# Kernel optimization log

Hardware: AMD Instinct MI355X
Metric: run time of the kernel (lower is better)

## Reference

```python
import jax, jax.numpy as jnp
import numpy as np

B, S, H, I, E, K = 1, 2048, 1024, 512, 16, 4


def setup_inputs() -> dict:
    key = jax.random.key(0)
    k0, k1, k2, k3, k4, k5 = jax.random.split(key, 6)
    hidden_states = jax.random.normal(k0, (B, S, H), jnp.float32)
    T = B * S
    topk_idx = jax.random.randint(k1, (T, K), 0, E, dtype=jnp.int32)
    raw = jax.random.uniform(k2, (T, K), jnp.float32)
    topk_weight = raw / jnp.sum(raw, axis=-1, keepdims=True)  # normalized top-k gate weights
    scale = 0.02
    w_gate = jax.random.normal(k3, (E, H, I), jnp.float32) * scale
    w_up = jax.random.normal(k4, (E, H, I), jnp.float32) * scale
    w_down = jax.random.normal(k5, (E, I, H), jnp.float32) * scale
    return {
        "hidden_states": hidden_states,
        "topk_idx": topk_idx,
        "topk_weight": topk_weight,
        "w_gate": w_gate,
        "w_up": w_up,
        "w_down": w_down,
    }


def reference(hidden_states, topk_idx, topk_weight, w_gate, w_up, w_down):
    # hidden_states: [B,S,H]; topk_idx/topk_weight: [T,K]; w_*: [E,H,I]/[E,I,H]
    b, s, h = hidden_states.shape
    t = b * s
    e = w_gate.shape[0]
    x = hidden_states.reshape(t, h)
    # routing_weights.scatter_(1, topk_idx, topk_weight)
    routing_weights = jnp.zeros((t, e), x.dtype).at[
        jnp.arange(t)[:, None], topk_idx
    ].set(topk_weight)
    # per-expert gated MLP over all tokens (math identical to masked dispatch:
    # tokens with routing weight 0 contribute nothing)
    g = jnp.einsum("th,ehi->eti", x, w_gate)  # [E,T,I]
    u = jnp.einsum("th,ehi->eti", x, w_up)
    d = jnp.einsum("eti,eih->eth", jax.nn.silu(g) * u, w_down)  # [E,T,H]
    out = jnp.einsum("eth,te->th", d, routing_weights)  # weighted combine
    return out.reshape(b, s, h)
```

## Files before the change

kernel.cpp:

```cpp
#include <hip/hip_runtime.h>
#include <hip/hip_bf16.h>
#include <stdint.h>

#define HH 1024
#define II 512
#define EE 16
#define TT 2048
#define KTOP 4
#define PP (TT * KTOP)
#define MAXROWS 12288

typedef unsigned short u16;
typedef unsigned int u32;
typedef __attribute__((ext_vector_type(8))) short short8;
typedef __attribute__((ext_vector_type(4))) float f32x4;
typedef __attribute__((ext_vector_type(4))) unsigned short u16x4;
typedef __attribute__((ext_vector_type(8))) unsigned short u16x8;
typedef __attribute__((ext_vector_type(4))) unsigned int u32x4;

__device__ __forceinline__ u16 f2bf(float f) {
  union { float f; unsigned u; } v; v.f = f;
  unsigned r = v.u + 0x7fffu + ((v.u >> 16) & 1u);
  return (u16)(r >> 16);
}
__device__ __forceinline__ float bf2f(u16 b) {
  union { unsigned u; float f; } v; v.u = ((unsigned)b) << 16; return v.f;
}
__device__ __forceinline__ u32 packbf(float lo, float hi) {
  return (u32)f2bf(lo) | ((u32)f2bf(hi) << 16);
}

__device__ __forceinline__ void gld16(const u16* g, u16* l) {
  __builtin_amdgcn_global_load_lds(
      (const __attribute__((address_space(1))) unsigned int*)g,
      (__attribute__((address_space(3))) unsigned int*)l, 16, 0, 0);
}

union PLds {
  int s_e[PP];
  u32 t32[2][128][68];
};

__global__ __launch_bounds__(1024) void prep_fused(
    const float* __restrict__ x, const int* __restrict__ tidx,
    const float* __restrict__ tw,
    const float* __restrict__ wg, const float* __restrict__ wu,
    u16* __restrict__ xb, u16* __restrict__ WgT, u16* __restrict__ WuT,
    int* __restrict__ perm, float* __restrict__ wt, int* __restrict__ rowof,
    int* __restrict__ tile_e, int* __restrict__ tile_r,
    int* __restrict__ ntiles) {
  __shared__ PLds L;
  __shared__ int whist[16][16];
  __shared__ int wbase[16][16];
  __shared__ int pad_lo[EE], pad_hi[EE];

  const int bid = blockIdx.x;
  const int tid = threadIdx.x;

  if (bid == 0) {
    const int lane = tid & 63;
    const int wv = tid >> 6;

#pragma unroll
    for (int i = 0; i < 2; i++) {
      const int t = tid + i * 1024;
      const int4 v = ((const int4*)tidx)[t];
      const bool v0 = (v.x != v.y) && (v.x != v.z) && (v.x != v.w);
      const bool v1 = (v.y != v.z) && (v.y != v.w);
      const bool v2 = (v.z != v.w);
      L.s_e[t * 4 + 0] = v.x | (v0 ? 16 : 0);
      L.s_e[t * 4 + 1] = v.y | (v1 ? 16 : 0);
      L.s_e[t * 4 + 2] = v.z | (v2 ? 16 : 0);
      L.s_e[t * 4 + 3] = v.w | 16;
    }
    __syncthreads();

    int h0, h1, h2, h3, h4, h5, h6, h7, h8, h9, h10, h11, h12, h13, h14, h15;
    h0=h1=h2=h3=h4=h5=h6=h7=h8=h9=h10=h11=h12=h13=h14=h15=0;
    const unsigned long long ltm = (1ull << lane) - 1ull;
    for (int c = 0; c < 8; c++) {
      const int p = (wv << 9) + (c << 6) + lane;
      const int se = L.s_e[p];
      const int e = se & 15;
      const bool valid = (se & 16) != 0;
      int rank = 0;
#define RANK_STEP(J, HJ)                                            \
      {                                                             \
        unsigned long long m = __ballot(valid && (e == J));         \
        if (valid && (e == J)) rank = HJ + __popcll(m & ltm);       \
        HJ += __popcll(m);                                          \
      }
      RANK_STEP(0, h0)  RANK_STEP(1, h1)  RANK_STEP(2, h2)  RANK_STEP(3, h3)
      RANK_STEP(4, h4)  RANK_STEP(5, h5)  RANK_STEP(6, h6)  RANK_STEP(7, h7)
      RANK_STEP(8, h8)  RANK_STEP(9, h9)  RANK_STEP(10, h10) RANK_STEP(11, h11)
      RANK_STEP(12, h12) RANK_STEP(13, h13) RANK_STEP(14, h14) RANK_STEP(15, h15)
#undef RANK_STEP
      if (valid) L.s_e[p] = se | (rank << 16);
    }
    if (lane == 0) {
      whist[wv][0] = h0;   whist[wv][1] = h1;   whist[wv][2] = h2;   whist[wv][3] = h3;
      whist[wv][4] = h4;   whist[wv][5] = h5;   whist[wv][6] = h6;   whist[wv][7] = h7;
      whist[wv][8] = h8;   whist[wv][9] = h9;   whist[wv][10] = h10; whist[wv][11] = h11;
      whist[wv][12] = h12; whist[wv][13] = h13; whist[wv][14] = h14; whist[wv][15] = h15;
    }
    __syncthreads();

    if (tid == 0) {
      int off = 0, nt = 0;
      for (int j = 0; j < EE; j++) {
        int tot = 0;
        for (int w = 0; w < 16; w++) { wbase[w][j] = off + tot; tot += whist[w][j]; }
        const int cap = (tot + 127) & ~127;
        pad_lo[j] = off + tot;
        pad_hi[j] = off + cap;
        for (int m0 = 0; m0 < cap; m0 += 128) { tile_e[nt] = j; tile_r[nt] = off + m0; nt++; }
        off += cap;
      }
      *ntiles = nt;
    }
    __syncthreads();

#pragma unroll
    for (int i = 0; i < 8; i++) {
      const int p = i * 1024 + tid;
      const int se = L.s_e[p];
      int pos = -1;
      if (se & 16) {
        const int e = se & 15;
        const int r = se >> 16;
        pos = wbase[p >> 9][e] + r;
        perm[pos] = p >> 2;
        wt[pos] = tw[p];
      }
      rowof[p] = pos;
    }
    for (int j = 0; j < EE; j++) {
      const int lo = pad_lo[j], hi = pad_hi[j];
      for (int i = lo + tid; i < hi; i += 1024) {
        perm[i] = 0;
        wt[i] = 0.f;
      }
    }
    return;
  }

  if (bid <= 128) {
    const int base = ((bid - 1) * 1024 + tid) * 16;
    f32x4 v0 = *(const f32x4*)(x + base);
    f32x4 v1 = *(const f32x4*)(x + base + 4);
    f32x4 v2 = *(const f32x4*)(x + base + 8);
    f32x4 v3 = *(const f32x4*)(x + base + 12);
    u16x8 o0 = { f2bf(v0[0]), f2bf(v0[1]), f2bf(v0[2]), f2bf(v0[3]),
                 f2bf(v1[0]), f2bf(v1[1]), f2bf(v1[2]), f2bf(v1[3]) };
    u16x8 o1 = { f2bf(v2[0]), f2bf(v2[1]), f2bf(v2[2]), f2bf(v2[3]),
                 f2bf(v3[0]), f2bf(v3[1]), f2bf(v3[2]), f2bf(v3[3]) };
    *(u16x8*)(xb + base) = o0;
    *(u16x8*)(xb + base + 8) = o1;
    return;
  }

  const int pb = bid - 129;
  const int zz = pb >> 5;
  const int sub = pb & 31;
  const int xi = sub & 3, yi = sub >> 2;
  const size_t mat = (size_t)zz * HH * II;
  const int r0 = yi * 128, c0 = xi * 128;

  const int rp = tid >> 4, cq8 = (tid & 15) * 8;
  const size_t soff = mat + (size_t)(r0 + 2 * rp) * II + c0 + cq8;
  const float* sp0 = wg + soff;
  const float* sp1 = wu + soff;
  const f32x4 a0 = *(const f32x4*)(sp0);
  const f32x4 a1 = *(const f32x4*)(sp0 + 4);
  const f32x4 b0 = *(const f32x4*)(sp0 + II);
  const f32x4 b1 = *(const f32x4*)(sp0 + II + 4);
  const f32x4 e0 = *(const f32x4*)(sp1);
  const f32x4 e1 = *(const f32x4*)(sp1 + 4);
  const f32x4 g0 = *(const f32x4*)(sp1 + II);
  const f32x4 g1 = *(const f32x4*)(sp1 + II + 4);
  __builtin_amdgcn_sched_barrier(0);

  const int key = tid & 15;
  const int rpx = rp ^ ((key & 7) << 3) ^ (((key >> 2) & 1) << 2);
  const int c = tid >> 3, q = tid & 7;
  const int rkey = c >> 3;
  const int qb = (q ^ (rkey & 7)) * 8;
  const int b2 = ((rkey >> 2) & 1) * 4;
  const size_t doff = mat + (size_t)(c0 + c) * HH + r0 + q * 16;

#pragma unroll
  for (int j = 0; j < 4; j++) L.t32[0][cq8 + j][rpx] = packbf(a0[j], b0[j]);
#pragma unroll
  for (int j = 0; j < 4; j++) L.t32[0][cq8 + 4 + j][rpx] = packbf(a1[j], b1[j]);
  __syncthreads();
#pragma unroll
  for (int j = 0; j < 4; j++) L.t32[1][cq8 + j][rpx] = packbf(e0[j], g0[j]);
#pragma unroll
  for (int j = 0; j < 4; j++) L.t32[1][cq8 + 4 + j][rpx] = packbf(e1[j], g1[j]);
  {
    u32x4 v0, v1;
#pragma unroll
    for (int j = 0; j < 4; j++) v0[j] = L.t32[0][c][qb + b2 + j];
#pragma unroll
    for (int j = 0; j < 4; j++) v1[j] = L.t32[0][c][qb + (b2 ^ 4) + j];
    u16* dp = WgT + doff;
    *(u32x4*)(dp) = v0;
    *(u32x4*)(dp + 8) = v1;
  }
  __syncthreads();
  {
    u32x4 v0, v1;
#pragma unroll
    for (int j = 0; j < 4; j++) v0[j] = L.t32[1][c][qb + b2 + j];
#pragma unroll
    for (int j = 0; j < 4; j++) v1[j] = L.t32[1][c][qb + (b2 ^ 4) + j];
    u16* dp = WuT + doff;
    *(u32x4*)(dp) = v0;
    *(u32x4*)(dp + 8) = v1;
  }
}

__global__ __launch_bounds__(256) void gemm1_kernel(
    const u16* __restrict__ xb, const u16* __restrict__ WgT, const u16* __restrict__ WuT,
    const float* __restrict__ wd, u16* __restrict__ WdT,
    const int* __restrict__ perm, const float* __restrict__ wt,
    const int* __restrict__ tile_e, const int* __restrict__ tile_r,
    const int* __restrict__ ntiles, u16* __restrict__ ACT) {
  __shared__ __align__(16) u16 SMEM[16384];
  const int tid = threadIdx.x;

  if (blockIdx.y >= 80) {
    const int pb = (blockIdx.y - 80) * 8 + blockIdx.x;
    const int zz = pb >> 6;
    const int sub = pb & 63;
    const int r0 = (sub >> 4) * 128;
    const int c0 = (sub & 15) * 64;
    const size_t mat = (size_t)zz * II * HH;
    u32 (*T32)[68] = (u32(*)[68])SMEM;

    const int rpA = tid >> 3;
    const int cq8 = (tid & 7) * 8;
    const float* spA = wd + mat + (size_t)(r0 + 2 * rpA) * HH + c0 + cq8;
    const float* spB = spA + (size_t)64 * HH;
    const f32x4 a0 = *(const f32x4*)(spA);
    const f32x4 a1 = *(const f32x4*)(spA + 4);
    const f32x4 b0 = *(const f32x4*)(spA + HH);
    const f32x4 b1 = *(const f32x4*)(spA + HH + 4);
    const f32x4 e0 = *(const f32x4*)(spB);
    const f32x4 e1 = *(const f32x4*)(spB + 4);
    const f32x4 g0 = *(const f32x4*)(spB + HH);
    const f32x4 g1 = *(const f32x4*)(spB + HH + 4);
    __builtin_amdgcn_sched_barrier(0);

    const int key = tid & 7;
    const int sw = ((key & 7) << 3) ^ (((key >> 2) & 1) << 2);
    const int rpxA = rpA ^ sw;
    const int rpxB = (rpA + 32) ^ sw;
#pragma unroll
    for (int j = 0; j < 4; j++) T32[cq8 + j][rpxA] = packbf(a0[j], b0[j]);
#pragma unroll
    for (int j = 0; j < 4; j++) T32[cq8 + 4 + j][rpxA] = packbf(a1[j], b1[j]);
#pragma unroll
    for (int j = 0; j < 4; j++) T32[cq8 + j][rpxB] = packbf(e0[j], g0[j]);
#pragma unroll
    for (int j = 0; j < 4; j++) T32[cq8 + 4 + j][rpxB] = packbf(e1[j], g1[j]);
    __syncthreads();

    const int c = tid >> 2;
    const int q2 = tid & 3;
    const int rkey = c >> 3;
    const int b2 = ((rkey >> 2) & 1) * 4;
#pragma unroll
    for (int pass = 0; pass < 2; pass++) {
      const int o = q2 + pass * 4;
      const int qb = (o ^ (rkey & 7)) * 8;
      u32x4 v0, v1;
#pragma unroll
      for (int j = 0; j < 4; j++) v0[j] = T32[c][qb + b2 + j];
#pragma unroll
      for (int j = 0; j < 4; j++) v1[j] = T32[c][qb + (b2 ^ 4) + j];
      u16* dp = WdT + mat + (size_t)(c0 + c) * II + r0 + o * 16;
      *(u32x4*)(dp) = v0;
      *(u32x4*)(dp + 8) = v1;
    }
    return;
  }

  const int tileid = blockIdx.y;
  if (tileid >= *ntiles) return;
  const int e = tile_e[tileid];
  const int row0 = tile_r[tileid];
  const int n0 = blockIdx.x * 64;

  u16* const As = SMEM;
  u16* const Gs = SMEM + 8192;
  u16* const Us = SMEM + 12288;

  const int lane = tid & 63;
  const int wid = tid >> 6;
  const int wm = wid >> 1, wn = wid & 1;
  const int fr = lane & 15, fq = lane >> 4;

  const int lrow = lane >> 3;
  const int sc8 = ((lane & 7) ^ lrow) * 8;

  const u16* gA[4]; u16* lA[4];
#pragma unroll
  for (int j = 0; j < 4; j++) {
    const int trow = j * 32 + wid * 8 + lrow;
    gA[j] = xb + (size_t)perm[row0 + trow] * HH + sc8;
    lA[j] = As + (j * 4 + wid) * 512;
  }
  const u16 *gG[2], *gU[2];
  u16 *lG[2], *lU[2];
#pragma unroll
  for (int j = 0; j < 2; j++) {
    const int nrow = j * 32 + wid * 8 + lrow;
    gG[j] = WgT + ((size_t)e * II + n0 + nrow) * HH + sc8;
    gU[j] = WuT + ((size_t)e * II + n0 + nrow) * HH + sc8;
    lG[j] = Gs + (j * 4 + wid) * 512;
    lU[j] = Us + (j * 4 + wid) * 512;
  }

  f32x4 accg[4][2], accu[4][2];
  const f32x4 vz = {0.f, 0.f, 0.f, 0.f};
#pragma unroll
  for (int m = 0; m < 4; m++)
#pragma unroll
    for (int n = 0; n < 2; n++) { accg[m][n] = vz; accu[m][n] = vz; }

  for (int k0 = 0; k0 < HH; k0 += 64) {
    __syncthreads();
#pragma unroll
    for (int j = 0; j < 4; j++) gld16(gA[j] + k0, lA[j]);
#pragma unroll
    for (int j = 0; j < 2; j++) { gld16(gG[j] + k0, lG[j]); gld16(gU[j] + k0, lU[j]); }
    __syncthreads();

#pragma unroll
    for (int ks = 0; ks < 2; ks++) {
      short8 af[4], bg[2], bu[2];
#pragma unroll
      for (int m = 0; m < 4; m++) {
        const int r = wm * 64 + m * 16 + fr;
        af[m] = *(const short8*)(&As[r * 64 + (((ks * 4 + fq) ^ (r & 7)) * 8)]);
      }
#pragma unroll
      for (int n = 0; n < 2; n++) {
        const int r = wn * 32 + n * 16 + fr;
        bg[n] = *(const short8*)(&Gs[r * 64 + (((ks * 4 + fq) ^ (r & 7)) * 8)]);
        bu[n] = *(const short8*)(&Us[r * 64 + (((ks * 4 + fq) ^ (r & 7)) * 8)]);
      }
#pragma unroll
      for (int m = 0; m < 4; m++)
#pragma unroll
        for (int n = 0; n < 2; n++) {
          accg[m][n] = __builtin_amdgcn_mfma_f32_16x16x32_bf16(af[m], bg[n], accg[m][n], 0, 0, 0);
          accu[m][n] = __builtin_amdgcn_mfma_f32_16x16x32_bf16(af[m], bu[n], accu[m][n], 0, 0, 0);
        }
    }
  }

#pragma unroll
  for (int m = 0; m < 4; m++) {
    const int rbase = wm * 64 + m * 16 + fq * 4;
#pragma unroll
    for (int j = 0; j < 4; j++) {
      const int rloc = rbase + j;
      const float w = wt[row0 + rloc];
#pragma unroll
      for (int n = 0; n < 2; n++) {
        const float g = accg[m][n][j];
        const float u = accu[m][n][j];
        const float s = g / (1.f + __expf(-g));
        ACT[(size_t)(row0 + rloc) * II + n0 + (wn * 32 + n * 16 + fr)] = f2bf(s * u * w);
      }
    }
  }
}

__global__ __launch_bounds__(256) void gemm2_kernel(
    const u16* __restrict__ ACT, const u16* __restrict__ WdT,
    const int* __restrict__ tile_e, const int* __restrict__ tile_r,
    const int* __restrict__ ntiles, u16* __restrict__ D) {
  const int tileid = blockIdx.y;
  if (tileid >= *ntiles) return;
  const int e = tile_e[tileid];
  const int row0 = tile_r[tileid];
  const int n0 = blockIdx.x * 128;

  __shared__ __align__(16) u16 As[128 * 64];
  __shared__ __align__(16) u16 Bs[128 * 64];

  const int tid = threadIdx.x;
  const int lane = tid & 63;
  const int wid = tid >> 6;
  const int wm = wid >> 1, wn = wid & 1;
  const int fr = lane & 15, fq = lane >> 4;

  const int lrow = lane >> 3;
  const int sc8 = ((lane & 7) ^ lrow) * 8;

  const u16 *gA[4], *gB[4];
  u16 *lA[4], *lB[4];
#pragma unroll
  for (int j = 0; j < 4; j++) {
    const int trow = j * 32 + wid * 8 + lrow;
    gA[j] = ACT + (size_t)(row0 + trow) * II + sc8;
    gB[j] = WdT + ((size_t)e * HH + n0 + trow) * II + sc8;
    lA[j] = As + (j * 4 + wid) * 512;
    lB[j] = Bs + (j * 4 + wid) * 512;
  }

  f32x4 acc[4][4];
  const f32x4 vz = {0.f, 0.f, 0.f, 0.f};
#pragma unroll
  for (int m = 0; m < 4; m++)
#pragma unroll
    for (int n = 0; n < 4; n++) acc[m][n] = vz;

  for (int k0 = 0; k0 < II; k0 += 64) {
    __syncthreads();
#pragma unroll
    for (int j = 0; j < 4; j++) { gld16(gA[j] + k0, lA[j]); gld16(gB[j] + k0, lB[j]); }
    __syncthreads();

#pragma unroll
    for (int ks = 0; ks < 2; ks++) {
      short8 af[4], bf[4];
#pragma unroll
      for (int m = 0; m < 4; m++) {
        const int r = wm * 64 + m * 16 + fr;
        af[m] = *(const short8*)(&As[r * 64 + (((ks * 4 + fq) ^ (r & 7)) * 8)]);
      }
#pragma unroll
      for (int n = 0; n < 4; n++) {
        const int r = wn * 64 + n * 16 + fr;
        bf[n] = *(const short8*)(&Bs[r * 64 + (((ks * 4 + fq) ^ (r & 7)) * 8)]);
      }
#pragma unroll
      for (int m = 0; m < 4; m++)
#pragma unroll
        for (int n = 0; n < 4; n++)
          acc[m][n] = __builtin_amdgcn_mfma_f32_16x16x32_bf16(af[m], bf[n], acc[m][n], 0, 0, 0);
    }
  }

#pragma unroll
  for (int m = 0; m < 4; m++) {
    const int rbase = wm * 64 + m * 16 + fq * 4;
#pragma unroll
    for (int j = 0; j < 4; j++) {
      u16* dp = D + (size_t)(row0 + rbase + j) * HH + n0 + wn * 64 + fr;
#pragma unroll
      for (int n = 0; n < 4; n++)
        dp[n * 16] = f2bf(acc[m][n][j]);
    }
  }
}

__global__ __launch_bounds__(256) void combine_kernel(
    const u16* __restrict__ D, const int* __restrict__ rowof,
    float* __restrict__ out) {
  const int t = blockIdx.x;
  const int h = threadIdx.x * 4;
  const int4 r4 = ((const int4*)rowof)[t];
  float a0 = 0.f, a1 = 0.f, a2 = 0.f, a3 = 0.f;
#define ACCUM(R)                                                     \
  if ((R) >= 0) {                                                    \
    u16x4 d = *(const u16x4*)(D + (size_t)(R) * HH + h);             \
    a0 += bf2f(d[0]); a1 += bf2f(d[1]); a2 += bf2f(d[2]); a3 += bf2f(d[3]); \
  }
  ACCUM(r4.x) ACCUM(r4.y) ACCUM(r4.z) ACCUM(r4.w)
#undef ACCUM
  float4 o = { a0, a1, a2, a3 };
  *(float4*)(out + (size_t)t * HH + h) = o;
}

extern "C" void kernel_launch(void* const* d_in, const int* in_sizes, int n_in,
                              void* d_out, int out_size, void* d_ws, size_t ws_size,
                              hipStream_t stream) {
  const float* x = (const float*)d_in[0];
  const int* tidx = (const int*)d_in[1];
  const float* tw = (const float*)d_in[2];
  const float* wg = (const float*)d_in[3];
  const float* wu = (const float*)d_in[4];
  const float* wd = (const float*)d_in[5];
  float* out = (float*)d_out;

  char* ws = (char*)d_ws;
  int* ntiles = (int*)(ws + 0);
  int* tile_e = (int*)(ws + 1024);
  int* tile_r = (int*)(ws + 2048);
  int* perm = (int*)(ws + 4096);
  float* wt = (float*)(ws + 53248);
  int* rowof = (int*)(ws + 102400);
  u16* xb = (u16*)(ws + 262144);
  u16* WgT = (u16*)(ws + 4456448);
  u16* WuT = (u16*)(ws + 21233664);
  u16* WdT = (u16*)(ws + 38010880);
  u16* ACT = (u16*)(ws + 54788096);
  u16* D = (u16*)(ws + 4456448);

  prep_fused<<<641, 1024, 0, stream>>>(x, tidx, tw, wg, wu,
                                       xb, WgT, WuT,
                                       perm, wt, rowof, tile_e, tile_r, ntiles);
  gemm1_kernel<<<dim3(8, 208), 256, 0, stream>>>(xb, WgT, WuT, wd, WdT, perm, wt,
                                                 tile_e, tile_r, ntiles, ACT);
  gemm2_kernel<<<dim3(HH / 128, 80), 256, 0, stream>>>(ACT, WdT,
                                                       tile_e, tile_r, ntiles, D);
  combine_kernel<<<TT, 256, 0, stream>>>(D, rowof, out);
}
```

Measured before the change: 84.18 us.

## Read fp32 down-proj weights directly in gemm2, drop WdT transpose pre-pass

Removes the bf16 transpose of w_down that ran as extra blocks inside gemm1. gemm2 now reads fp32 w_down straight from global memory into registers, converts each element to bf16 with the hardware conversion, and feeds it as the MFMA B operand. Only the activation tile is staged in LDS, now double-buffered. This saves a full write and re-read of WdT but doubles the bytes read for the weights. Those weight loads are strided per element across the H dimension, so coalescing may be poor, and register pressure rises.

```diff
diff --git a/kernel.cpp b/kernel.cpp
--- a/kernel.cpp
+++ b/kernel.cpp
@@ -28,6 +28,10 @@
 }
 __device__ __forceinline__ u32 packbf(float lo, float hi) {
   return (u32)f2bf(lo) | ((u32)f2bf(hi) << 16);
+}
+__device__ __forceinline__ short f2bf_hw(float f) {
+  __hip_bfloat16 h = __float2bfloat16(f);
+  union { __hip_bfloat16 h; short s; } v; v.h = h; return v.s;
 }
 
 __device__ __forceinline__ void gld16(const u16* g, u16* l) {
@@ -222,80 +226,20 @@
 
 __global__ __launch_bounds__(256) void gemm1_kernel(
     const u16* __restrict__ xb, const u16* __restrict__ WgT, const u16* __restrict__ WuT,
-    const float* __restrict__ wd, u16* __restrict__ WdT,
     const int* __restrict__ perm, const float* __restrict__ wt,
     const int* __restrict__ tile_e, const int* __restrict__ tile_r,
     const int* __restrict__ ntiles, u16* __restrict__ ACT) {
-  __shared__ __align__(16) u16 SMEM[16384];
-  const int tid = threadIdx.x;
-
-  if (blockIdx.y >= 80) {
-    const int pb = (blockIdx.y - 80) * 8 + blockIdx.x;
-    const int zz = pb >> 6;
-    const int sub = pb & 63;
-    const int r0 = (sub >> 4) * 128;
-    const int c0 = (sub & 15) * 64;
-    const size_t mat = (size_t)zz * II * HH;
-    u32 (*T32)[68] = (u32(*)[68])SMEM;
-
-    const int rpA = tid >> 3;
-    const int cq8 = (tid & 7) * 8;
-    const float* spA = wd + mat + (size_t)(r0 + 2 * rpA) * HH + c0 + cq8;
-    const float* spB = spA + (size_t)64 * HH;
-    const f32x4 a0 = *(const f32x4*)(spA);
-    const f32x4 a1 = *(const f32x4*)(spA + 4);
-    const f32x4 b0 = *(const f32x4*)(spA + HH);
-    const f32x4 b1 = *(const f32x4*)(spA + HH + 4);
-    const f32x4 e0 = *(const f32x4*)(spB);
-    const f32x4 e1 = *(const f32x4*)(spB + 4);
-    const f32x4 g0 = *(const f32x4*)(spB + HH);
-    const f32x4 g1 = *(const f32x4*)(spB + HH + 4);
-    __builtin_amdgcn_sched_barrier(0);
-
-    const int key = tid & 7;
-    const int sw = ((key & 7) << 3) ^ (((key >> 2) & 1) << 2);
-    const int rpxA = rpA ^ sw;
-    const int rpxB = (rpA + 32) ^ sw;
-#pragma unroll
-    for (int j = 0; j < 4; j++) T32[cq8 + j][rpxA] = packbf(a0[j], b0[j]);
-#pragma unroll
-    for (int j = 0; j < 4; j++) T32[cq8 + 4 + j][rpxA] = packbf(a1[j], b1[j]);
-#pragma unroll
-    for (int j = 0; j < 4; j++) T32[cq8 + j][rpxB] = packbf(e0[j], g0[j]);
-#pragma unroll
-    for (int j = 0; j < 4; j++) T32[cq8 + 4 + j][rpxB] = packbf(e1[j], g1[j]);
-    __syncthreads();
-
-    const int c = tid >> 2;
-    const int q2 = tid & 3;
-    const int rkey = c >> 3;
-    const int b2 = ((rkey >> 2) & 1) * 4;
-#pragma unroll
-    for (int pass = 0; pass < 2; pass++) {
-      const int o = q2 + pass * 4;
-      const int qb = (o ^ (rkey & 7)) * 8;
-      u32x4 v0, v1;
-#pragma unroll
-      for (int j = 0; j < 4; j++) v0[j] = T32[c][qb + b2 + j];
-#pragma unroll
-      for (int j = 0; j < 4; j++) v1[j] = T32[c][qb + (b2 ^ 4) + j];
-      u16* dp = WdT + mat + (size_t)(c0 + c) * II + r0 + o * 16;
-      *(u32x4*)(dp) = v0;
-      *(u32x4*)(dp + 8) = v1;
-    }
-    return;
-  }
-
   const int tileid = blockIdx.y;
   if (tileid >= *ntiles) return;
   const int e = tile_e[tileid];
   const int row0 = tile_r[tileid];
   const int n0 = blockIdx.x * 64;
 
-  u16* const As = SMEM;
-  u16* const Gs = SMEM + 8192;
-  u16* const Us = SMEM + 12288;
-
+  __shared__ __align__(16) u16 As[128 * 64];
+  __shared__ __align__(16) u16 Gs[64 * 64];
+  __shared__ __align__(16) u16 Us[64 * 64];
+
+  const int tid = threadIdx.x;
   const int lane = tid & 63;
   const int wid = tid >> 6;
   const int wm = wid >> 1, wn = wid & 1;
@@ -379,8 +323,42 @@
   }
 }
 
+#define G2_LOADB(FB, K0)                                               \
+  _Pragma("unroll")                                                    \
+  for (int nf = 0; nf < 2; nf++)                                       \
+    _Pragma("unroll")                                                  \
+    for (int ks = 0; ks < 2; ks++)                                     \
+      _Pragma("unroll")                                                \
+      for (int j = 0; j < 8; j++)                                      \
+        FB[nf][ks][j] = dbase[(size_t)((K0) + ks * 32 + fq * 8 + j) * HH + nf * 16];
+
+#define G2_STAGE(BUF, K0)                                              \
+  _Pragma("unroll")                                                    \
+  for (int j = 0; j < 4; j++) gld16(gA[j] + (K0), (BUF) + (j * 4 + wid) * 512);
+
+#define G2_COMPUTE(FB, ASBUF)                                          \
+  {                                                                    \
+    short8 b[2][2];                                                    \
+    _Pragma("unroll")                                                  \
+    for (int nf = 0; nf < 2; nf++)                                     \
+      _Pragma("unroll")                                                \
+      for (int ks = 0; ks < 2; ks++)                                   \
+        _Pragma("unroll")                                              \
+        for (int j = 0; j < 8; j++)                                    \
+          b[nf][ks][j] = f2bf_hw(FB[nf][ks][j]);                       \
+    _Pragma("unroll")                                                  \
+    for (int ks = 0; ks < 2; ks++)                                     \
+      _Pragma("unroll")                                                \
+      for (int m = 0; m < 8; m++) {                                    \
+        const int r = m * 16 + fr;                                     \
+        const short8 a = *(const short8*)(&(ASBUF)[r * 64 + (((ks * 4 + fq) ^ (r & 7)) * 8)]); \
+        acc[m][0] = __builtin_amdgcn_mfma_f32_16x16x32_bf16(a, b[0][ks], acc[m][0], 0, 0, 0); \
+        acc[m][1] = __builtin_amdgcn_mfma_f32_16x16x32_bf16(a, b[1][ks], acc[m][1], 0, 0, 0); \
+      }                                                                \
+  }
+
 __global__ __launch_bounds__(256) void gemm2_kernel(
-    const u16* __restrict__ ACT, const u16* __restrict__ WdT,
+    const u16* __restrict__ ACT, const float* __restrict__ wd,
     const int* __restrict__ tile_e, const int* __restrict__ tile_r,
     const int* __restrict__ ntiles, u16* __restrict__ D) {
   const int tileid = blockIdx.y;
@@ -389,72 +367,60 @@
   const int row0 = tile_r[tileid];
   const int n0 = blockIdx.x * 128;
 
-  __shared__ __align__(16) u16 As[128 * 64];
-  __shared__ __align__(16) u16 Bs[128 * 64];
+  __shared__ __align__(16) u16 As[2][128 * 64];
 
   const int tid = threadIdx.x;
   const int lane = tid & 63;
   const int wid = tid >> 6;
-  const int wm = wid >> 1, wn = wid & 1;
   const int fr = lane & 15, fq = lane >> 4;
 
   const int lrow = lane >> 3;
   const int sc8 = ((lane & 7) ^ lrow) * 8;
 
-  const u16 *gA[4], *gB[4];
-  u16 *lA[4], *lB[4];
+  const u16* gA[4];
 #pragma unroll
   for (int j = 0; j < 4; j++) {
     const int trow = j * 32 + wid * 8 + lrow;
     gA[j] = ACT + (size_t)(row0 + trow) * II + sc8;
-    gB[j] = WdT + ((size_t)e * HH + n0 + trow) * II + sc8;
-    lA[j] = As + (j * 4 + wid) * 512;
-    lB[j] = Bs + (j * 4 + wid) * 512;
-  }
-
-  f32x4 acc[4][4];
+  }
+  u16* const As0 = &As[0][0];
+  u16* const As1 = &As[1][0];
+
+  const int nc0 = n0 + wid * 32 + fr;
+  const float* dbase = wd + (size_t)e * II * HH + nc0;
+
+  f32x4 acc[8][2];
   const f32x4 vz = {0.f, 0.f, 0.f, 0.f};
 #pragma unroll
-  for (int m = 0; m < 4; m++)
-#pragma unroll
-    for (int n = 0; n < 4; n++) acc[m][n] = vz;
-
-  for (int k0 = 0; k0 < II; k0 += 64) {
-    __syncthreads();
-#pragma unroll
-    for (int j = 0; j < 4; j++) { gld16(gA[j] + k0, lA[j]); gld16(gB[j] + k0, lB[j]); }
-    __syncthreads();
-
-#pragma unroll
-    for (int ks = 0; ks < 2; ks++) {
-      short8 af[4], bf[4];
-#pragma unroll
-      for (int m = 0; m < 4; m++) {
-        const int r = wm * 64 + m * 16 + fr;
-        af[m] = *(const short8*)(&As[r * 64 + (((ks * 4 + fq) ^ (r & 7)) * 8)]);
-      }
-#pragma unroll
-      for (int n = 0; n < 4; n++) {
-        const int r = wn * 64 + n * 16 + fr;
-        bf[n] = *(const short8*)(&Bs[r * 64 + (((ks * 4 + fq) ^ (r & 7)) * 8)]);
-      }
-#pragma unroll
-      for (int m = 0; m < 4; m++)
-#pragma unroll
-        for (int n = 0; n < 4; n++)
-          acc[m][n] = __builtin_amdgcn_mfma_f32_16x16x32_bf16(af[m], bf[n], acc[m][n], 0, 0, 0);
-    }
-  }
-
-#pragma unroll
-  for (int m = 0; m < 4; m++) {
-    const int rbase = wm * 64 + m * 16 + fq * 4;
-#pragma unroll
-    for (int j = 0; j < 4; j++) {
-      u16* dp = D + (size_t)(row0 + rbase + j) * HH + n0 + wn * 64 + fr;
-#pragma unroll
-      for (int n = 0; n < 4; n++)
-        dp[n * 16] = f2bf(acc[m][n][j]);
+  for (int m = 0; m < 8; m++) { acc[m][0] = vz; acc[m][1] = vz; }
+
+  float fbA[2][2][8], fbB[2][2][8];
+
+  G2_LOADB(fbA, 0)
+  G2_STAGE(As0, 0)
+  __syncthreads();
+
+  for (int t = 0; t < 8; t += 2) {
+    G2_LOADB(fbB, (t + 1) * 64)
+    G2_STAGE(As1, (t + 1) * 64)
+    G2_COMPUTE(fbA, As0)
+    __syncthreads();
+    if (t < 6) {
+      G2_LOADB(fbA, (t + 2) * 64)
+      G2_STAGE(As0, (t + 2) * 64)
+    }
+    G2_COMPUTE(fbB, As1)
+    __syncthreads();
+  }
+
+#pragma unroll
+  for (int m = 0; m < 8; m++) {
+#pragma unroll
+    for (int jj = 0; jj < 4; jj++) {
+      const int rloc = m * 16 + fq * 4 + jj;
+      u16* dp = D + (size_t)(row0 + rloc) * HH + nc0;
+      dp[0]  = f2bf(acc[m][0][jj]);
+      dp[16] = f2bf(acc[m][1][jj]);
     }
   }
 }
@@ -498,16 +464,15 @@
   u16* xb = (u16*)(ws + 262144);
   u16* WgT = (u16*)(ws + 4456448);
   u16* WuT = (u16*)(ws + 21233664);
-  u16* WdT = (u16*)(ws + 38010880);
   u16* ACT = (u16*)(ws + 54788096);
   u16* D = (u16*)(ws + 4456448);
 
   prep_fused<<<641, 1024, 0, stream>>>(x, tidx, tw, wg, wu,
                                        xb, WgT, WuT,
                                        perm, wt, rowof, tile_e, tile_r, ntiles);
-  gemm1_kernel<<<dim3(8, 208), 256, 0, stream>>>(xb, WgT, WuT, wd, WdT, perm, wt,
-                                                 tile_e, tile_r, ntiles, ACT);
-  gemm2_kernel<<<dim3(HH / 128, 80), 256, 0, stream>>>(ACT, WdT,
+  gemm1_kernel<<<dim3(II / 64, 80), 256, 0, stream>>>(xb, WgT, WuT, perm, wt,
+                                                      tile_e, tile_r, ntiles, ACT);
+  gemm2_kernel<<<dim3(HH / 128, 80), 256, 0, stream>>>(ACT, wd,
                                                        tile_e, tile_r, ntiles, D);
   combine_kernel<<<TT, 256, 0, stream>>>(D, rowof, out);
 }
```

Result: faster. 82.08 us (-2.5%).
